# Optimization experiments

Measured on AMD Instinct MI355X. Metric: run time of the kernel, lower is better.

Reference implementation:

```python
import jax, jax.numpy as jnp
import numpy as np

B, N, INTER, RNN, W = 256, 128, 128, 128, 8


def _rms(x):
    # x / sqrt(mean(x^2, dim=2))
    return x / jnp.sqrt(jnp.mean(x * x, axis=2, keepdims=True))


def _sage(x, src, dst, deg, wl, bl, wr):
    # PyG SAGEConv(mean aggr, normalize=True): lin_l(mean_j x_j) + lin_r(x), then L2-normalize.
    # edge_index from torch.combinations(arange(k),2).t(): src=row0 (i<j), dst=row1;
    # batch repeat duplicates edges without node offsets -> mean unchanged, only nodes <N aggregate.
    agg = jax.ops.segment_sum(x[src], dst, num_segments=x.shape[0]) / deg[:, None]
    out = agg @ wl.T + bl + x @ wr.T
    nrm = jnp.maximum(jnp.linalg.norm(out, axis=-1, keepdims=True), 1e-12)
    return out / nrm


def setup_inputs() -> dict:
    key = jax.random.key(0)
    ks = jax.random.split(key, 32)
    g = lambda i, shape: jax.random.normal(ks[i], shape, dtype=jnp.float32) * 0.05
    return {
        'flows': jax.random.normal(ks[0], (B, N, N), dtype=jnp.float32),
        'coords_emb': jax.random.normal(ks[1], (B, N, 2 * N), dtype=jnp.float32),
        # Encoder_Coords: 4 pointwise Conv1d layers (kernel=1 == per-token Linear)
        'cw1': g(2, (INTER, 2 * N)), 'cb1': g(3, (INTER,)),
        'cw2': g(4, (2 * INTER, INTER)), 'cb2': g(5, (2 * INTER,)),
        'cw3': g(6, (RNN, 2 * INTER)), 'cb3': g(7, (RNN,)),
        'cw4': g(8, (RNN, RNN)), 'cb4': g(9, (RNN,)),
        # Encoder_Flows: 4 SAGEConv layers (lin_l with bias, lin_r no bias)
        'g1_wl': g(10, (INTER, N)), 'g1_bl': g(11, (INTER,)), 'g1_wr': g(12, (INTER, N)),
        'g2_wl': g(13, (2 * INTER, INTER)), 'g2_bl': g(14, (2 * INTER,)), 'g2_wr': g(15, (2 * INTER, INTER)),
        'g3_wl': g(16, (INTER, 2 * INTER)), 'g3_bl': g(17, (INTER,)), 'g3_wr': g(18, (INTER, 2 * INTER)),
        'g4_wl': g(19, (RNN, INTER)), 'g4_bl': g(20, (RNN,)), 'g4_wr': g(21, (RNN, INTER)),
        # Worker: per-worker Q/K projections (bias=False), stacked [W, out, in]
        'qca': g(22, (W, RNN, RNN)), 'kca': g(23, (W, RNN, RNN)),
        'qsa': g(24, (W, RNN, RNN)), 'ksa': g(25, (W, RNN, RNN)),
        # s_1s[0], s_2s[0]: Linear(N*W -> N, bias=False)
        's1w': g(26, (N, N * W)), 's2w': g(27, (N, N * W)),
    }


def reference(flows, coords_emb, cw1, cb1, cw2, cb2, cw3, cb3, cw4, cb4,
              g1_wl, g1_bl, g1_wr, g2_wl, g2_bl, g2_wr, g3_wl, g3_bl, g3_wr,
              g4_wl, g4_bl, g4_wr, qca, kca, qsa, ksa, s1w, s2w):
    # ---- rms_norm inputs (Model.action) ----
    f_in = _rms(flows)
    c_in = _rms(coords_emb)

    # ---- Encoder_Flows: SAGE stack over flattened [B*N, N] nodes ----
    x = f_in.reshape(-1, N)                      # [B*N, N]
    src, dst = jnp.triu_indices(N, k=1)          # combinations(arange(N), r=2)
    deg = jnp.maximum(
        jax.ops.segment_sum(jnp.ones_like(src, dtype=x.dtype), dst, num_segments=x.shape[0]), 1.0)
    x = _sage(x, src, dst, deg, g1_wl, g1_bl, g1_wr)
    x = _sage(x, src, dst, deg, g2_wl, g2_bl, g2_wr)
    x = _sage(x, src, dst, deg, g3_wl, g3_bl, g3_wr)
    x = _sage(x, src, dst, deg, g4_wl, g4_bl, g4_wr)
    f = _rms(jax.nn.relu(x).reshape(B, N, RNN))

    # ---- Encoder_Coords: 4 pointwise convs (no nonlinearity), attn=False ----
    c = c_in @ cw1.T + cb1
    c = c @ cw2.T + cb2
    c = c @ cw3.T + cb3
    c = c @ cw4.T + cb4
    c = _rms(c)

    # ---- Worker (dropout=0.0 -> identity) ----
    scale = jnp.sqrt(jnp.float32(RNN))
    # cross-attention branch (result discarded by Worker.forward, kept for fidelity)
    Qc = jnp.einsum('bnd,wod->bwno', f, qca)
    Kc = jnp.einsum('bmd,wod->bwmo', c, kca)
    ca = jnp.einsum('bwno,bwmo->bwnm', Qc, Kc) / scale
    ca = ca.transpose(0, 2, 3, 1).reshape(B, N, N * W) @ s1w.T  # [B,N,N], unused
    # self-attention branch (returned)
    Qs = jnp.einsum('bnd,wod->bwno', f, qsa)
    Ks = jnp.einsum('bmd,wod->bwmo', f, ksa)
    sa = jnp.einsum('bwno,bwmo->bwnm', Qs, Ks) / scale          # [B,W,N,N]
    sa = sa.transpose(0, 2, 3, 1).reshape(B, N, N * W) @ s2w.T  # [B,N,N]
    return sa
```

## Files before the change

kernel.cpp:

```cpp
#include <hip/hip_runtime.h>
#include <math.h>


typedef __attribute__((ext_vector_type(8))) short bf16x8;
typedef __attribute__((ext_vector_type(4))) float f32x4;

__device__ inline ushort f2b(float x) {
  unsigned u = __builtin_bit_cast(unsigned, x);
  unsigned r = (u + 0x7fffu + ((u >> 16) & 1u)) >> 16;
  return (ushort)r;
}
__device__ inline int ftswz(int e) { return ((e & 7) ^ ((e >> 3) & 15)) << 4; }

__device__ inline void ctr_signal(unsigned* c) {
  __threadfence();
  __syncthreads();
  if (threadIdx.x == 0)
    __hip_atomic_fetch_add(c, 1u, __ATOMIC_RELEASE, __HIP_MEMORY_SCOPE_AGENT);
}
__device__ inline void ctr_wait(unsigned* c, unsigned tgt) {
  if (threadIdx.x == 0) {
    while (__hip_atomic_load(c, __ATOMIC_ACQUIRE, __HIP_MEMORY_SCOPE_AGENT) < tgt)
      __builtin_amdgcn_s_sleep(8);
  }
  __syncthreads();
}

__global__ __launch_bounds__(256) void prep_all_k(
    const float* __restrict__ s2w,
    const float* __restrict__ wl1, const float* __restrict__ wl2,
    const float* __restrict__ wl3, const float* __restrict__ wl4,
    const float* __restrict__ wr1, const float* __restrict__ wr2,
    const float* __restrict__ wr3, const float* __restrict__ wr4,
    ushort* __restrict__ SBp, ushort* __restrict__ WL, ushort* __restrict__ WR,
    ushort* __restrict__ WRp, float* __restrict__ SS, unsigned* __restrict__ CTR) {
  if (blockIdx.x == 0) {
    SS[threadIdx.x] = 0.f;
    SS[threadIdx.x + 256] = 0.f;
    if (threadIdx.x < 8) CTR[threadIdx.x] = 0u;
  }
  int i = blockIdx.x * 256 + threadIdx.x;
  if (i < 131072) {
    int w = i >> 14, p = (i >> 7) & 127, m = i & 127;
    int sidx = ((((w * 2 + (p >> 6)) * 4 + ((p >> 4) & 3)) * 4 + (m >> 5)) * 64 +
                ((m >> 3) & 3) * 16 + (p & 15)) * 8 + (m & 7);
    SBp[sidx] = f2b(s2w[p * 1024 + m * 8 + w]);
    return;
  }
  i -= 131072;
  if (i < 98304) {
    float v, u;
    int base, K, col, k;
    if (i < 16384)      { v = wl1[i];         u = wr1[i];         base = 0;     K = 128; col = i >> 7;            k = i & 127; }
    else if (i < 49152) { int j = i - 16384;  v = wl2[j]; u = wr2[j]; base = 16384; K = 128; col = j >> 7;       k = j & 127; }
    else if (i < 81920) { int j = i - 49152;  v = wl3[j]; u = wr3[j]; base = 49152; K = 256; col = j >> 8;       k = j & 255; }
    else                { int j = i - 81920;  v = wl4[j]; u = wr4[j]; base = 81920; K = 128; col = j >> 7;       k = j & 127; }
    WL[i] = f2b(v);
    ushort ub = f2b(u);
    WR[i] = ub;
    int pidx = base + (((col >> 4) * (K / 32) + (k >> 5)) * 64 +
                       ((k >> 3) & 3) * 16 + (col & 15)) * 8 + (k & 7);
    WRp[pidx] = ub;
  }
}

template <int K, int N, int MODE>
__device__ void chain_dev(char* XS, char* C0T, float* sArr,
                          const float* __restrict__ flows, const ushort* __restrict__ XTsrc,
                          const float* __restrict__ SSprev,
                          const ushort* __restrict__ Wl, const ushort* __restrict__ Wr,
                          const float* __restrict__ bias,
                          ushort* __restrict__ XTdst, float* __restrict__ YTdst,
                          float* __restrict__ SScur, int cbid) {
  const int tid = threadIdx.x;
  const int lane = tid & 63, wv = tid >> 6, lr = lane & 15, lg = lane >> 4;
  const int cG0 = cbid * 16;

  if (MODE == 0) {
    #pragma unroll
    for (int it = 0; it < 16; ++it) {
      int idx = tid + it * 256;
      int row = idx >> 5, c4 = idx & 31;
      const float4 v = *reinterpret_cast<const float4*>(flows + (size_t)row * 128 + c4 * 4);
      float ss = v.x * v.x + v.y * v.y + v.z * v.z + v.w * v.w;
      ss += __shfl_xor(ss, 16); ss += __shfl_xor(ss, 8);
      ss += __shfl_xor(ss, 4);  ss += __shfl_xor(ss, 2); ss += __shfl_xor(ss, 1);
      *reinterpret_cast<ushort*>(XS + (c4 * 4 + 0) * 272 + row * 2) = f2b(v.x);
      *reinterpret_cast<ushort*>(XS + (c4 * 4 + 1) * 272 + row * 2) = f2b(v.y);
      *reinterpret_cast<ushort*>(XS + (c4 * 4 + 2) * 272 + row * 2) = f2b(v.z);
      *reinterpret_cast<ushort*>(XS + (c4 * 4 + 3) * 272 + row * 2) = f2b(v.w);
      if ((tid & 31) == 0) sArr[row] = rsqrtf(ss * (1.0f / 128.0f));
    }
  } else {
    for (int e = tid * 8; e < K * 128; e += 2048) {
      uint4 v = *reinterpret_cast<const uint4*>(XTsrc + e);
      *reinterpret_cast<uint4*>(XS + (e >> 7) * 272 + (e & 127) * 2) = v;
    }
    if (tid < 128) sArr[tid] = 1.0f / fmaxf(sqrtf(SSprev[tid]), 1e-12f);
  }
  __syncthreads();

  bf16x8 a[2][K / 32];
  float sr[2][4];
  #pragma unroll
  for (int mt = 0; mt < 2; ++mt) {
    int R = wv * 32 + mt * 16 + lr;
    #pragma unroll
    for (int ks = 0; ks < K / 32; ++ks) {
      union { ushort us[8]; bf16x8 v; } u;
      #pragma unroll
      for (int j = 0; j < 8; ++j)
        u.us[j] = *reinterpret_cast<const ushort*>(XS + (ks * 32 + lg * 8 + j) * 272 + R * 2);
      a[mt][ks] = u.v;
    }
    #pragma unroll
    for (int rr = 0; rr < 4; ++rr) sr[mt][rr] = sArr[wv * 32 + mt * 16 + 4 * lg + rr];
  }

  bf16x8 aL[2][4];
  #pragma unroll
  for (int mt = 0; mt < 2; ++mt) {
    int rowL = wv * 32 + mt * 16 + lr;
    ushort iv = f2b(1.0f / (float)(rowL > 1 ? rowL : 1));
    #pragma unroll
    for (int ks = 0; ks < 4; ++ks)
      #pragma unroll
      for (int j = 0; j < 8; ++j) {
        int k = ks * 32 + lg * 8 + j;
        aL[mt][ks][j] = (short)((k < rowL) ? iv : 0);
      }
  }

  const int cG = cG0 + lr;
  {
    bf16x8 bw[K / 32];
    #pragma unroll
    for (int ks = 0; ks < K / 32; ++ks)
      bw[ks] = *reinterpret_cast<const bf16x8*>(Wl + (size_t)cG * K + ks * 32 + lg * 8);
    #pragma unroll
    for (int mt = 0; mt < 2; ++mt) {
      f32x4 acc = {0.f, 0.f, 0.f, 0.f};
      #pragma unroll
      for (int ks = 0; ks < K / 32; ++ks)
        acc = __builtin_amdgcn_mfma_f32_16x16x32_bf16(a[mt][ks], bw[ks], acc, 0, 0, 0);
      int m0 = wv * 32 + mt * 16 + lg * 4;
      uint2 pk;
      pk.x = (unsigned)f2b(acc[0] * sr[mt][0]) | ((unsigned)f2b(acc[1] * sr[mt][1]) << 16);
      pk.y = (unsigned)f2b(acc[2] * sr[mt][2]) | ((unsigned)f2b(acc[3] * sr[mt][3]) << 16);
      *reinterpret_cast<uint2*>(C0T + lr * 256 + ((2 * m0) ^ ((lr & 7) << 4))) = pk;
    }
  }
  __syncthreads();

  {
    bf16x8 bc[4], bw[K / 32];
    #pragma unroll
    for (int ks = 0; ks < 4; ++ks)
      bc[ks] = *reinterpret_cast<const bf16x8*>(C0T + lr * 256 + ((ks * 64 + lg * 16) ^ ((lr & 7) << 4)));
    #pragma unroll
    for (int ks = 0; ks < K / 32; ++ks)
      bw[ks] = *reinterpret_cast<const bf16x8*>(Wr + (size_t)cG * K + ks * 32 + lg * 8);
    float bb = bias[cG];
    #pragma unroll
    for (int mt = 0; mt < 2; ++mt) {
      f32x4 cacc = {0.f, 0.f, 0.f, 0.f}, acc = {0.f, 0.f, 0.f, 0.f};
      #pragma unroll
      for (int ks = 0; ks < 4; ++ks)
        cacc = __builtin_amdgcn_mfma_f32_16x16x32_bf16(aL[mt][ks], bc[ks], cacc, 0, 0, 0);
      #pragma unroll
      for (int ks = 0; ks < K / 32; ++ks)
        acc = __builtin_amdgcn_mfma_f32_16x16x32_bf16(a[mt][ks], bw[ks], acc, 0, 0, 0);
      int m0 = wv * 32 + mt * 16 + lg * 4;
      float ssq[4];
      if (MODE < 2) {
        float y0 = acc[0] * sr[mt][0] + bb + cacc[0];
        float y1 = acc[1] * sr[mt][1] + bb + cacc[1];
        float y2 = acc[2] * sr[mt][2] + bb + cacc[2];
        float y3 = acc[3] * sr[mt][3] + bb + cacc[3];
        uint2 pk;
        pk.x = (unsigned)f2b(y0) | ((unsigned)f2b(y1) << 16);
        pk.y = (unsigned)f2b(y2) | ((unsigned)f2b(y3) << 16);
        *reinterpret_cast<uint2*>(&XTdst[(size_t)cG * 128 + m0]) = pk;
        ssq[0] = y0 * y0; ssq[1] = y1 * y1; ssq[2] = y2 * y2; ssq[3] = y3 * y3;
      } else {
        float4 vv;
        vv.x = fmaxf(acc[0] * sr[mt][0] + bb + cacc[0], 0.f);
        vv.y = fmaxf(acc[1] * sr[mt][1] + bb + cacc[1], 0.f);
        vv.z = fmaxf(acc[2] * sr[mt][2] + bb + cacc[2], 0.f);
        vv.w = fmaxf(acc[3] * sr[mt][3] + bb + cacc[3], 0.f);
        *reinterpret_cast<float4*>(&YTdst[(size_t)cG * 128 + m0]) = vv;
        ssq[0] = vv.x * vv.x; ssq[1] = vv.y * vv.y; ssq[2] = vv.z * vv.z; ssq[3] = vv.w * vv.w;
      }
      #pragma unroll
      for (int rr = 0; rr < 4; ++rr) {
        float ss = ssq[rr];
        ss += __shfl_xor(ss, 1); ss += __shfl_xor(ss, 2);
        ss += __shfl_xor(ss, 4); ss += __shfl_xor(ss, 8);
        if (lr == 0) atomicAdd(&SScur[m0 + rr], ss);
      }
    }
  }
}

__device__ inline void stage_flows_nb(const float* __restrict__ flows, int blk,
                                      char* A_, float* sArr, int wv, int lane) {
  int r2 = lane >> 5;
  int c4 = lane & 31;
  #pragma unroll
  for (int it = 0; it < 8; ++it) {
    int rowbase = wv * 16 + it * 2;
    const float4 v = *reinterpret_cast<const float4*>(
        flows + ((size_t)blk * 64 + rowbase) * 128 + lane * 4);
    int row = rowbase + r2;
    float ss = v.x * v.x + v.y * v.y + v.z * v.z + v.w * v.w;
    ss += __shfl_xor(ss, 16); ss += __shfl_xor(ss, 8);
    ss += __shfl_xor(ss, 4);  ss += __shfl_xor(ss, 2); ss += __shfl_xor(ss, 1);
    uint2 pk;
    pk.x = (unsigned)f2b(v.x) | ((unsigned)f2b(v.y) << 16);
    pk.y = (unsigned)f2b(v.z) | ((unsigned)f2b(v.w) << 16);
    *reinterpret_cast<uint2*>(A_ + row * 256 + ((c4 * 8) ^ ((row & 7) << 4))) = pk;
    if (c4 == 0) sArr[row] = rsqrtf(ss * (1.0f / 128.0f));
  }
}

template <int K, int N>
__device__ inline void sage_layer_nb(const char* Xsrc, char* Xdst,
                                     const float* sP, float* sN,
                                     const ushort* __restrict__ Wrp,
                                     const float* __restrict__ bias,
                                     int wv, int lr, int lg, int l64) {
  bf16x8 a[K / 32];
  float sr[4];
  int rowA = wv * 16 + lr;
  #pragma unroll
  for (int ks = 0; ks < K / 32; ++ks)
    a[ks] = *reinterpret_cast<const bf16x8*>(
        Xsrc + rowA * (K * 2) + ((ks * 64 + lg * 16) ^ ((rowA & 7) << 4)));
  #pragma unroll
  for (int rr = 0; rr < 4; ++rr) sr[rr] = sP[wv * 16 + 4 * lg + rr];
  float ssq[4] = {0.f, 0.f, 0.f, 0.f};
  #pragma unroll
  for (int nt = 0; nt < N / 16; ++nt) {
    int col = nt * 16 + lr;
    bf16x8 b[K / 32];
    #pragma unroll
    for (int ks = 0; ks < K / 32; ++ks)
      b[ks] = *reinterpret_cast<const bf16x8*>(Wrp + (((size_t)nt * (K / 32) + ks) * 64 + l64) * 8);
    f32x4 acc = {0.f, 0.f, 0.f, 0.f};
    #pragma unroll
    for (int ks = 0; ks < K / 32; ++ks)
      acc = __builtin_amdgcn_mfma_f32_16x16x32_bf16(a[ks], b[ks], acc, 0, 0, 0);
    float bb = bias[col];
    #pragma unroll
    for (int rr = 0; rr < 4; ++rr) {
      int row = wv * 16 + 4 * lg + rr;
      float y = acc[rr] * sr[rr] + bb;
      *reinterpret_cast<ushort*>(Xdst + row * (N * 2) + ((col * 2) ^ ((row & 7) << 4))) = f2b(y);
      ssq[rr] += y * y;
    }
  }
  #pragma unroll
  for (int rr = 0; rr < 4; ++rr) {
    float ss = ssq[rr];
    ss += __shfl_xor(ss, 1); ss += __shfl_xor(ss, 2);
    ss += __shfl_xor(ss, 4); ss += __shfl_xor(ss, 8);
    if (lr == 0) sN[wv * 16 + 4 * lg + rr] = 1.0f / fmaxf(sqrtf(ss), 1e-12f);
  }
}

__device__ inline void sage_layer_last_nb(const char* Xsrc, const float* sP,
                                          const ushort* __restrict__ Wrp,
                                          const float* __restrict__ bias,
                                          int wv, int lr, int lg, int l64,
                                          ushort* __restrict__ Fg, int blk) {
  bf16x8 a[4];
  float sr[4];
  int rowA = wv * 16 + lr;
  #pragma unroll
  for (int ks = 0; ks < 4; ++ks)
    a[ks] = *reinterpret_cast<const bf16x8*>(
        Xsrc + rowA * 256 + ((ks * 64 + lg * 16) ^ ((rowA & 7) << 4)));
  #pragma unroll
  for (int rr = 0; rr < 4; ++rr) sr[rr] = sP[wv * 16 + 4 * lg + rr];
  float yreg[8][4];
  float ssq[4] = {0.f, 0.f, 0.f, 0.f};
  #pragma unroll
  for (int nt = 0; nt < 8; ++nt) {
    int col = nt * 16 + lr;
    bf16x8 b[4];
    #pragma unroll
    for (int ks = 0; ks < 4; ++ks)
      b[ks] = *reinterpret_cast<const bf16x8*>(Wrp + (((size_t)nt * 4 + ks) * 64 + l64) * 8);
    f32x4 acc = {0.f, 0.f, 0.f, 0.f};
    #pragma unroll
    for (int ks = 0; ks < 4; ++ks)
      acc = __builtin_amdgcn_mfma_f32_16x16x32_bf16(a[ks], b[ks], acc, 0, 0, 0);
    float bb = bias[col];
    #pragma unroll
    for (int rr = 0; rr < 4; ++rr) {
      float y = acc[rr] * sr[rr] + bb;
      yreg[nt][rr] = y;
      float v = fmaxf(y, 0.f);
      ssq[rr] += v * v;
    }
  }
  float sc[4];
  #pragma unroll
  for (int rr = 0; rr < 4; ++rr) {
    float ss = ssq[rr];
    ss += __shfl_xor(ss, 1); ss += __shfl_xor(ss, 2);
    ss += __shfl_xor(ss, 4); ss += __shfl_xor(ss, 8);
    sc[rr] = sqrtf(128.0f / fmaxf(ss, 1e-20f));
  }
  #pragma unroll
  for (int nt = 0; nt < 8; ++nt)
    #pragma unroll
    for (int rr = 0; rr < 4; ++rr) {
      int row = wv * 16 + 4 * lg + rr;
      Fg[((size_t)blk * 64 + row) * 128 + nt * 16 + lr] = f2b(fmaxf(yreg[nt][rr], 0.f) * sc[rr]);
    }
}

__global__ __launch_bounds__(256, 2) void mega2_k(
    const float* __restrict__ flows,
    const float* __restrict__ qsa, const float* __restrict__ ksa,
    const ushort* __restrict__ WL, const ushort* __restrict__ WR,
    const ushort* __restrict__ WRp,
    const float* __restrict__ bl1, const float* __restrict__ bl2,
    const float* __restrict__ bl3, const float* __restrict__ bl4,
    ushort* __restrict__ Fg, ushort* __restrict__ MBT,
    ushort* __restrict__ XT1, ushort* __restrict__ XT2, ushort* __restrict__ XT3,
    float* __restrict__ YT4, float* __restrict__ SS, unsigned* __restrict__ CTR) {
  __shared__ char L[74240];
  const int bid = blockIdx.x;
  const int tid = threadIdx.x;
  const int lane = tid & 63, wv = tid >> 6, lr = lane & 15, lg = lane >> 4;

  if (bid < 16) {
    char* XS = L;
    char* C0T = L + 69632;
    float* sArr = (float*)(L + 73728);
    int cbid = bid;
    if (cbid < 8) {
      chain_dev<128, 128, 0>(XS, C0T, sArr, flows, nullptr, nullptr,
                             WL + 0, WR + 0, bl1, XT1, nullptr, SS + 0, cbid);
      ctr_signal(&CTR[0]);
    }
    ctr_wait(&CTR[0], 8);
    chain_dev<128, 256, 1>(XS, C0T, sArr, nullptr, XT1, SS + 0,
                           WL + 16384, WR + 16384, bl2, XT2, nullptr, SS + 128, cbid);
    ctr_signal(&CTR[1]);
    ctr_wait(&CTR[1], 16);
    if (cbid < 8) {
      chain_dev<256, 128, 1>(XS, C0T, sArr, nullptr, XT2, SS + 128,
                             WL + 49152, WR + 49152, bl3, XT3, nullptr, SS + 256, cbid);
      ctr_signal(&CTR[2]);
    }
    ctr_wait(&CTR[2], 8);
    if (cbid < 8) {
      chain_dev<128, 128, 2>(XS, C0T, sArr, nullptr, XT3, SS + 256,
                             WL + 81920, WR + 81920, bl4, nullptr, YT4, SS + 384, cbid);
      ctr_signal(&CTR[3]);
    }
    ctr_wait(&CTR[3], 8);
    if (cbid < 8) {
      int t = cbid * 256 + tid;
      int r = t >> 4, cs = t & 15;
      float sc = sqrtf(128.0f / fmaxf(SS[384 + r], 1e-20f));
      ushort tmp[8];
      #pragma unroll
      for (int j = 0; j < 8; ++j) {
        int c = cs * 8 + j;
        tmp[j] = f2b(YT4[(size_t)c * 128 + r] * sc);
      }
      *reinterpret_cast<uint4*>(&Fg[(size_t)r * 128 + cs * 8]) = *reinterpret_cast<uint4*>(tmp);
    }
    return;
  }

  if (bid < 24) {
    char* QT  = L;
    char* KTm = L + 32768;
    int w = bid - 16;
    const float* qw = qsa + (size_t)w * 16384;
    const float* kw = ksa + (size_t)w * 16384;
    for (int e = tid; e < 16384; e += 256) {
      int op = e >> 7, c = e & 127;
      int off = c * 256 + ((op * 2) ^ ((c & 7) << 4));
      *reinterpret_cast<ushort*>(QT + off)  = f2b(qw[e]);
      *reinterpret_cast<ushort*>(KTm + off) = f2b(kw[e]);
    }
    __syncthreads();
    #pragma unroll
    for (int rt = 0; rt < 2; ++rt) {
      int e = wv * 32 + rt * 16 + lr;
      bf16x8 a[4];
      #pragma unroll
      for (int ks = 0; ks < 4; ++ks)
        a[ks] = *reinterpret_cast<const bf16x8*>(KTm + e * 256 + ((ks * 64 + lg * 16) ^ ((e & 7) << 4)));
      #pragma unroll
      for (int ct = 0; ct < 8; ++ct) {
        int d = ct * 16 + lr;
        bf16x8 bq[4];
        #pragma unroll
        for (int ks = 0; ks < 4; ++ks)
          bq[ks] = *reinterpret_cast<const bf16x8*>(QT + d * 256 + ((ks * 64 + lg * 16) ^ ((d & 7) << 4)));
        f32x4 acc = {0.f, 0.f, 0.f, 0.f};
        #pragma unroll
        for (int ks = 0; ks < 4; ++ks)
          acc = __builtin_amdgcn_mfma_f32_16x16x32_bf16(a[ks], bq[ks], acc, 0, 0, 0);
        uint2 pk;
        pk.x = (unsigned)f2b(acc[0]) | ((unsigned)f2b(acc[1]) << 16);
        pk.y = (unsigned)f2b(acc[2]) | ((unsigned)f2b(acc[3]) << 16);
        size_t base = ((((size_t)ct * 8 + w) * 4 + wv) * 64 +
                       (size_t)(((rt * 2 + (lg >> 1)) & 3) * 16 + lr)) * 8 + (lg & 1) * 4;
        *reinterpret_cast<uint2*>(&MBT[base]) = pk;
      }
    }
    return;
  }

  char* A_ = L;
  char* B_ = L + 16384;
  char* C_ = L + 32768;
  float* sA = (float*)(L + 65536);
  float* sB = (float*)(L + 65792);
  const int l64 = lane;
  int blk = bid - 24 + 2;
  stage_flows_nb(flows, blk, A_, sA, wv, lane);
  asm volatile("" ::: "memory");
  sage_layer_nb<128, 128>(A_, B_, sA, sB, WRp + 0,     bl1, wv, lr, lg, l64);
  asm volatile("" ::: "memory");
  sage_layer_nb<128, 256>(B_, C_, sB, sA, WRp + 16384, bl2, wv, lr, lg, l64);
  asm volatile("" ::: "memory");
  sage_layer_nb<256, 128>(C_, A_, sA, sB, WRp + 49152, bl3, wv, lr, lg, l64);
  asm volatile("" ::: "memory");
  sage_layer_last_nb(A_, sB, WRp + 81920, bl4, wv, lr, lg, l64, Fg, blk);
}

__global__ __launch_bounds__(512, 4) void attn_fused(
    const ushort* __restrict__ F, const ushort* __restrict__ MBT,
    const ushort* __restrict__ SBp, float* __restrict__ Out) {
  __shared__ char FT[32768];
  __shared__ char RTb[32768];

  const int bq = blockIdx.x;
  const int b = bq >> 1, ph = bq & 1;
  const int tid = threadIdx.x;
  const int l = tid & 63, wv = tid >> 6;
  const int lr = l & 15, lg = l >> 4;

  const ushort* Fb = F + (size_t)b * 16384;

  #pragma unroll
  for (int it = 0; it < 4; ++it) {
    int idx = tid + it * 512;
    int m = idx >> 4, eg = idx & 15;
    uint4 v = *reinterpret_cast<const uint4*>(Fb + m * 128 + eg * 8);
    const ushort* pv = reinterpret_cast<const ushort*>(&v);
    #pragma unroll
    for (int j = 0; j < 8; ++j) {
      int e = eg * 8 + j;
      *reinterpret_cast<ushort*>(FT + e * 256 + ((m * 2) ^ ftswz(e))) = pv[j];
    }
  }

  bf16x8 fa[4];
  {
    int n = wv * 16 + lr;
    #pragma unroll
    for (int ks = 0; ks < 4; ++ks)
      fa[ks] = *reinterpret_cast<const bf16x8*>(Fb + n * 128 + ks * 32 + lg * 8);
  }
  __syncthreads();

  bf16x8 af[4];
  {
    int e = wv * 16 + lr;
    #pragma unroll
    for (int ks = 0; ks < 4; ++ks)
      af[ks] = *reinterpret_cast<const bf16x8*>(
          FT + e * 256 + ((ks * 64 + lg * 16) ^ ftswz(e)));
  }

  f32x4 zacc[4];
  #pragma unroll
  for (int pt = 0; pt < 4; ++pt) zacc[pt] = f32x4{0.f, 0.f, 0.f, 0.f};

  const int eb0 = 2 * (wv * 16 + lg * 4);

  auto Rphase = [&](int w, char* RT) {
    #pragma unroll
    for (int pt = 0; pt < 4; ++pt) {
      int p = pt * 16 + lr;
      bf16x8 bs[4];
      #pragma unroll
      for (int ks = 0; ks < 4; ++ks)
        bs[ks] = *reinterpret_cast<const bf16x8*>(
            SBp + ((((size_t)(w * 2 + ph) * 4 + pt) * 4 + ks) * 64 + l) * 8);
      f32x4 rr = {0.f, 0.f, 0.f, 0.f};
      #pragma unroll
      for (int ks = 0; ks < 4; ++ks)
        rr = __builtin_amdgcn_mfma_f32_16x16x32_bf16(af[ks], bs[ks], rr, 0, 0, 0);
      uint2 pk;
      pk.x = (unsigned)f2b(rr[0]) | ((unsigned)f2b(rr[1]) << 16);
      pk.y = (unsigned)f2b(rr[2]) | ((unsigned)f2b(rr[3]) << 16);
      *reinterpret_cast<uint2*>(RT + p * 256 + (eb0 ^ ((p & 7) << 4))) = pk;
    }
  };
  auto Zphase = [&](int w, const char* RT) {
    bf16x8 mf[4];
    #pragma unroll
    for (int ks = 0; ks < 4; ++ks)
      mf[ks] = *reinterpret_cast<const bf16x8*>(
          MBT + ((((size_t)wv * 8 + w) * 4 + ks) * 64 + l) * 8);
    #pragma unroll
    for (int pt = 0; pt < 4; ++pt) {
      int p = pt * 16 + lr;
      bf16x8 bg[4];
      #pragma unroll
      for (int ks = 0; ks < 4; ++ks)
        bg[ks] = *reinterpret_cast<const bf16x8*>(
            RT + p * 256 + ((ks * 64 + lg * 16) ^ ((p & 7) << 4)));
      #pragma unroll
      for (int ks = 0; ks < 4; ++ks)
        zacc[pt] = __builtin_amdgcn_mfma_f32_16x16x32_bf16(mf[ks], bg[ks], zacc[pt], 0, 0, 0);
    }
  };

  Rphase(0, RTb);
  __syncthreads();
  #pragma unroll
  for (int w = 0; w < 7; ++w) {
    Zphase(w, RTb + (w & 1) * 16384);
    Rphase(w + 1, RTb + ((w + 1) & 1) * 16384);
    __syncthreads();
  }
  Zphase(7, RTb + 16384);
  #pragma unroll
  for (int pt = 0; pt < 4; ++pt) {
    int p = pt * 16 + lr;
    uint2 pk;
    pk.x = (unsigned)f2b(zacc[pt][0]) | ((unsigned)f2b(zacc[pt][1]) << 16);
    pk.y = (unsigned)f2b(zacc[pt][2]) | ((unsigned)f2b(zacc[pt][3]) << 16);
    *reinterpret_cast<uint2*>(RTb + p * 256 + (eb0 ^ ((p & 7) << 4))) = pk;
  }
  __syncthreads();

  const float inv_scale = 0.08838834764831845f;
  float* ob = Out + (size_t)b * 16384 + ph * 64;
  #pragma unroll
  for (int pt = 0; pt < 4; ++pt) {
    int p = pt * 16 + lr;
    bf16x8 bz[4];
    #pragma unroll
    for (int ks = 0; ks < 4; ++ks)
      bz[ks] = *reinterpret_cast<const bf16x8*>(
          RTb + p * 256 + ((ks * 64 + lg * 16) ^ ((p & 7) << 4)));
    f32x4 oa = {0.f, 0.f, 0.f, 0.f};
    #pragma unroll
    for (int ks = 0; ks < 4; ++ks)
      oa = __builtin_amdgcn_mfma_f32_16x16x32_bf16(fa[ks], bz[ks], oa, 0, 0, 0);
    int n0 = wv * 16 + lg * 4;
    #pragma unroll
    for (int r = 0; r < 4; ++r)
      ob[(size_t)(n0 + r) * 128 + p] = oa[r] * inv_scale;
  }
}

extern "C" void kernel_launch(void* const* d_in, const int* in_sizes, int n_in,
                              void* d_out, int out_size, void* d_ws, size_t ws_size,
                              hipStream_t stream) {
  const float* flows = (const float*)d_in[0];
  const float* g1_wl = (const float*)d_in[10];
  const float* g1_bl = (const float*)d_in[11];
  const float* g1_wr = (const float*)d_in[12];
  const float* g2_wl = (const float*)d_in[13];
  const float* g2_bl = (const float*)d_in[14];
  const float* g2_wr = (const float*)d_in[15];
  const float* g3_wl = (const float*)d_in[16];
  const float* g3_bl = (const float*)d_in[17];
  const float* g3_wr = (const float*)d_in[18];
  const float* g4_wl = (const float*)d_in[19];
  const float* g4_bl = (const float*)d_in[20];
  const float* g4_wr = (const float*)d_in[21];
  const float* qsa   = (const float*)d_in[24];
  const float* ksa   = (const float*)d_in[25];
  const float* s2w   = (const float*)d_in[27];
  float* out = (float*)d_out;
  char* wsb  = (char*)d_ws;

  ushort* FB16 = (ushort*)(wsb);
  ushort* SBp  = (ushort*)(wsb + 8388608);
  ushort* WL   = (ushort*)(wsb + 8650752);
  ushort* WR   = (ushort*)(wsb + 8847360);
  ushort* MBT  = (ushort*)(wsb + 9043968);
  ushort* XT1  = (ushort*)(wsb + 9306112);
  ushort* XT2  = (ushort*)(wsb + 9338880);
  ushort* XT3  = (ushort*)(wsb + 9404416);
  float*  YT4  = (float*)(wsb + 9437184);
  float*  SS   = (float*)(wsb + 9502720);
  ushort* WRp  = (ushort*)(wsb + 9504768);
  unsigned* CTR = (unsigned*)(wsb + 9701376);

  prep_all_k<<<896, 256, 0, stream>>>(s2w,
                                      g1_wl, g2_wl, g3_wl, g4_wl,
                                      g1_wr, g2_wr, g3_wr, g4_wr,
                                      SBp, WL, WR, WRp, SS, CTR);
  mega2_k<<<534, 256, 0, stream>>>(flows, qsa, ksa, WL, WR, WRp,
                                   g1_bl, g2_bl, g3_bl, g4_bl,
                                   FB16, MBT, XT1, XT2, XT3, YT4, SS, CTR);
  attn_fused<<<512, 512, 0, stream>>>(FB16, MBT, SBp, out);
}
```

Before: 86.75 us.

## Cut mega kernel shared memory to fit three blocks per CU

```diff
diff --git a/kernel.cpp b/kernel.cpp
--- a/kernel.cpp
+++ b/kernel.cpp
@@ -11,6 +11,7 @@
   return (ushort)r;
 }
 __device__ inline int ftswz(int e) { return ((e & 7) ^ ((e >> 3) & 15)) << 4; }
+__device__ inline int cAddrRow(int rl) { return (rl < 8) ? rl * 512 : 8192 + (rl - 8) * 512; }
 
 __device__ inline void ctr_signal(unsigned* c) {
   __threadfence();
@@ -74,47 +75,67 @@
                           float* __restrict__ SScur, int cbid) {
   const int tid = threadIdx.x;
   const int lane = tid & 63, wv = tid >> 6, lr = lane & 15, lg = lane >> 4;
-  const int cG0 = cbid * 16;
-
-  if (MODE == 0) {
-    #pragma unroll
-    for (int it = 0; it < 16; ++it) {
-      int idx = tid + it * 256;
-      int row = idx >> 5, c4 = idx & 31;
-      const float4 v = *reinterpret_cast<const float4*>(flows + (size_t)row * 128 + c4 * 4);
-      float ss = v.x * v.x + v.y * v.y + v.z * v.z + v.w * v.w;
-      ss += __shfl_xor(ss, 16); ss += __shfl_xor(ss, 8);
-      ss += __shfl_xor(ss, 4);  ss += __shfl_xor(ss, 2); ss += __shfl_xor(ss, 1);
-      *reinterpret_cast<ushort*>(XS + (c4 * 4 + 0) * 272 + row * 2) = f2b(v.x);
-      *reinterpret_cast<ushort*>(XS + (c4 * 4 + 1) * 272 + row * 2) = f2b(v.y);
-      *reinterpret_cast<ushort*>(XS + (c4 * 4 + 2) * 272 + row * 2) = f2b(v.z);
-      *reinterpret_cast<ushort*>(XS + (c4 * 4 + 3) * 272 + row * 2) = f2b(v.w);
-      if ((tid & 31) == 0) sArr[row] = rsqrtf(ss * (1.0f / 128.0f));
-    }
-  } else {
-    for (int e = tid * 8; e < K * 128; e += 2048) {
-      uint4 v = *reinterpret_cast<const uint4*>(XTsrc + e);
-      *reinterpret_cast<uint4*>(XS + (e >> 7) * 272 + (e & 127) * 2) = v;
-    }
-    if (tid < 128) sArr[tid] = 1.0f / fmaxf(sqrtf(SSprev[tid]), 1e-12f);
-  }
-  __syncthreads();
-
-  bf16x8 a[2][K / 32];
+  const int cG = cbid * 16 + lr;
+  constexpr int NH = K / 128;
+
   float sr[2][4];
-  #pragma unroll
-  for (int mt = 0; mt < 2; ++mt) {
-    int R = wv * 32 + mt * 16 + lr;
-    #pragma unroll
-    for (int ks = 0; ks < K / 32; ++ks) {
-      union { ushort us[8]; bf16x8 v; } u;
-      #pragma unroll
-      for (int j = 0; j < 8; ++j)
-        u.us[j] = *reinterpret_cast<const ushort*>(XS + (ks * 32 + lg * 8 + j) * 272 + R * 2);
-      a[mt][ks] = u.v;
-    }
-    #pragma unroll
-    for (int rr = 0; rr < 4; ++rr) sr[mt][rr] = sArr[wv * 32 + mt * 16 + 4 * lg + rr];
+  f32x4 acc1[2] = {{0.f,0.f,0.f,0.f},{0.f,0.f,0.f,0.f}};
+  f32x4 acc2[2] = {{0.f,0.f,0.f,0.f},{0.f,0.f,0.f,0.f}};
+
+  #pragma unroll
+  for (int h = 0; h < NH; ++h) {
+    __syncthreads();
+    if (MODE == 0) {
+      #pragma unroll
+      for (int it = 0; it < 16; ++it) {
+        int idx = tid + it * 256;
+        int row = idx >> 5, c4 = idx & 31;
+        const float4 v = *reinterpret_cast<const float4*>(flows + (size_t)row * 128 + c4 * 4);
+        float ss = v.x * v.x + v.y * v.y + v.z * v.z + v.w * v.w;
+        ss += __shfl_xor(ss, 16); ss += __shfl_xor(ss, 8);
+        ss += __shfl_xor(ss, 4);  ss += __shfl_xor(ss, 2); ss += __shfl_xor(ss, 1);
+        *reinterpret_cast<ushort*>(XS + (c4 * 4 + 0) * 272 + row * 2) = f2b(v.x);
+        *reinterpret_cast<ushort*>(XS + (c4 * 4 + 1) * 272 + row * 2) = f2b(v.y);
+        *reinterpret_cast<ushort*>(XS + (c4 * 4 + 2) * 272 + row * 2) = f2b(v.z);
+        *reinterpret_cast<ushort*>(XS + (c4 * 4 + 3) * 272 + row * 2) = f2b(v.w);
+        if ((tid & 31) == 0) sArr[row] = rsqrtf(ss * (1.0f / 128.0f));
+      }
+    } else {
+      for (int e = tid * 8; e < 16384; e += 2048) {
+        uint4 v = *reinterpret_cast<const uint4*>(XTsrc + h * 16384 + e);
+        *reinterpret_cast<uint4*>(XS + (e >> 7) * 272 + (e & 127) * 2) = v;
+      }
+      if (h == 0 && tid < 128) sArr[tid] = 1.0f / fmaxf(sqrtf(SSprev[tid]), 1e-12f);
+    }
+    __syncthreads();
+
+    #pragma unroll
+    for (int mt = 0; mt < 2; ++mt) {
+      int R = wv * 32 + mt * 16 + lr;
+      bf16x8 a[4];
+      #pragma unroll
+      for (int ks = 0; ks < 4; ++ks) {
+        union { ushort us[8]; bf16x8 v; } u;
+        #pragma unroll
+        for (int j = 0; j < 8; ++j)
+          u.us[j] = *reinterpret_cast<const ushort*>(XS + (ks * 32 + lg * 8 + j) * 272 + R * 2);
+        a[ks] = u.v;
+      }
+      if (h == 0) {
+        #pragma unroll
+        for (int rr = 0; rr < 4; ++rr) sr[mt][rr] = sArr[wv * 32 + mt * 16 + 4 * lg + rr];
+      }
+      #pragma unroll
+      for (int ks = 0; ks < 4; ++ks) {
+        bf16x8 bw = *reinterpret_cast<const bf16x8*>(Wl + (size_t)cG * K + h * 128 + ks * 32 + lg * 8);
+        acc1[mt] = __builtin_amdgcn_mfma_f32_16x16x32_bf16(a[ks], bw, acc1[mt], 0, 0, 0);
+      }
+      #pragma unroll
+      for (int ks = 0; ks < 4; ++ks) {
+        bf16x8 bw = *reinterpret_cast<const bf16x8*>(Wr + (size_t)cG * K + h * 128 + ks * 32 + lg * 8);
+        acc2[mt] = __builtin_amdgcn_mfma_f32_16x16x32_bf16(a[ks], bw, acc2[mt], 0, 0, 0);
+      }
+    }
   }
 
   bf16x8 aL[2][4];
@@ -131,52 +152,35 @@
       }
   }
 
-  const int cG = cG0 + lr;
+  #pragma unroll
+  for (int mt = 0; mt < 2; ++mt) {
+    int m0 = wv * 32 + mt * 16 + lg * 4;
+    uint2 pk;
+    pk.x = (unsigned)f2b(acc1[mt][0] * sr[mt][0]) | ((unsigned)f2b(acc1[mt][1] * sr[mt][1]) << 16);
+    pk.y = (unsigned)f2b(acc1[mt][2] * sr[mt][2]) | ((unsigned)f2b(acc1[mt][3] * sr[mt][3]) << 16);
+    *reinterpret_cast<uint2*>(C0T + lr * 256 + ((2 * m0) ^ ((lr & 7) << 4))) = pk;
+  }
+  __syncthreads();
+
   {
-    bf16x8 bw[K / 32];
-    #pragma unroll
-    for (int ks = 0; ks < K / 32; ++ks)
-      bw[ks] = *reinterpret_cast<const bf16x8*>(Wl + (size_t)cG * K + ks * 32 + lg * 8);
+    bf16x8 bc[4];
+    #pragma unroll
+    for (int ks = 0; ks < 4; ++ks)
+      bc[ks] = *reinterpret_cast<const bf16x8*>(C0T + lr * 256 + ((ks * 64 + lg * 16) ^ ((lr & 7) << 4)));
+    float bb = (MODE < 2) ? bias[cG] : bias[cG];
     #pragma unroll
     for (int mt = 0; mt < 2; ++mt) {
-      f32x4 acc = {0.f, 0.f, 0.f, 0.f};
-      #pragma unroll
-      for (int ks = 0; ks < K / 32; ++ks)
-        acc = __builtin_amdgcn_mfma_f32_16x16x32_bf16(a[mt][ks], bw[ks], acc, 0, 0, 0);
-      int m0 = wv * 32 + mt * 16 + lg * 4;
-      uint2 pk;
-      pk.x = (unsigned)f2b(acc[0] * sr[mt][0]) | ((unsigned)f2b(acc[1] * sr[mt][1]) << 16);
-      pk.y = (unsigned)f2b(acc[2] * sr[mt][2]) | ((unsigned)f2b(acc[3] * sr[mt][3]) << 16);
-      *reinterpret_cast<uint2*>(C0T + lr * 256 + ((2 * m0) ^ ((lr & 7) << 4))) = pk;
-    }
-  }
-  __syncthreads();
-
-  {
-    bf16x8 bc[4], bw[K / 32];
-    #pragma unroll
-    for (int ks = 0; ks < 4; ++ks)
-      bc[ks] = *reinterpret_cast<const bf16x8*>(C0T + lr * 256 + ((ks * 64 + lg * 16) ^ ((lr & 7) << 4)));
-    #pragma unroll
-    for (int ks = 0; ks < K / 32; ++ks)
-      bw[ks] = *reinterpret_cast<const bf16x8*>(Wr + (size_t)cG * K + ks * 32 + lg * 8);
-    float bb = bias[cG];
-    #pragma unroll
-    for (int mt = 0; mt < 2; ++mt) {
-      f32x4 cacc = {0.f, 0.f, 0.f, 0.f}, acc = {0.f, 0.f, 0.f, 0.f};
+      f32x4 cacc = {0.f, 0.f, 0.f, 0.f};
       #pragma unroll
       for (int ks = 0; ks < 4; ++ks)
         cacc = __builtin_amdgcn_mfma_f32_16x16x32_bf16(aL[mt][ks], bc[ks], cacc, 0, 0, 0);
-      #pragma unroll
-      for (int ks = 0; ks < K / 32; ++ks)
-        acc = __builtin_amdgcn_mfma_f32_16x16x32_bf16(a[mt][ks], bw[ks], acc, 0, 0, 0);
       int m0 = wv * 32 + mt * 16 + lg * 4;
       float ssq[4];
       if (MODE < 2) {
-        float y0 = acc[0] * sr[mt][0] + bb + cacc[0];
-        float y1 = acc[1] * sr[mt][1] + bb + cacc[1];
-        float y2 = acc[2] * sr[mt][2] + bb + cacc[2];
-        float y3 = acc[3] * sr[mt][3] + bb + cacc[3];
+        float y0 = acc2[mt][0] * sr[mt][0] + bb + cacc[0];
+        float y1 = acc2[mt][1] * sr[mt][1] + bb + cacc[1];
+        float y2 = acc2[mt][2] * sr[mt][2] + bb + cacc[2];
+        float y3 = acc2[mt][3] * sr[mt][3] + bb + cacc[3];
         uint2 pk;
         pk.x = (unsigned)f2b(y0) | ((unsigned)f2b(y1) << 16);
         pk.y = (unsigned)f2b(y2) | ((unsigned)f2b(y3) << 16);
@@ -184,10 +188,10 @@
         ssq[0] = y0 * y0; ssq[1] = y1 * y1; ssq[2] = y2 * y2; ssq[3] = y3 * y3;
       } else {
         float4 vv;
-        vv.x = fmaxf(acc[0] * sr[mt][0] + bb + cacc[0], 0.f);
-        vv.y = fmaxf(acc[1] * sr[mt][1] + bb + cacc[1], 0.f);
-        vv.z = fmaxf(acc[2] * sr[mt][2] + bb + cacc[2], 0.f);
-        vv.w = fmaxf(acc[3] * sr[mt][3] + bb + cacc[3], 0.f);
+        vv.x = fmaxf(acc2[mt][0] * sr[mt][0] + bb + cacc[0], 0.f);
+        vv.y = fmaxf(acc2[mt][1] * sr[mt][1] + bb + cacc[1], 0.f);
+        vv.z = fmaxf(acc2[mt][2] * sr[mt][2] + bb + cacc[2], 0.f);
+        vv.w = fmaxf(acc2[mt][3] * sr[mt][3] + bb + cacc[3], 0.f);
         *reinterpret_cast<float4*>(&YTdst[(size_t)cG * 128 + m0]) = vv;
         ssq[0] = vv.x * vv.x; ssq[1] = vv.y * vv.y; ssq[2] = vv.z * vv.z; ssq[3] = vv.w * vv.w;
       }
@@ -202,60 +206,59 @@
   }
 }
 
-__device__ inline void stage_flows_nb(const float* __restrict__ flows, int blk,
-                                      char* A_, float* sArr, int wv, int lane) {
+__device__ inline void sage_stage(const float* __restrict__ flows, int blk,
+                                  char* W, float* sArr, int wv, int lane) {
   int r2 = lane >> 5;
   int c4 = lane & 31;
   #pragma unroll
   for (int it = 0; it < 8; ++it) {
-    int rowbase = wv * 16 + it * 2;
+    int rl0 = it * 2;
     const float4 v = *reinterpret_cast<const float4*>(
-        flows + ((size_t)blk * 64 + rowbase) * 128 + lane * 4);
-    int row = rowbase + r2;
+        flows + ((size_t)blk * 64 + wv * 16 + rl0) * 128 + lane * 4);
+    int rl = rl0 + r2;
     float ss = v.x * v.x + v.y * v.y + v.z * v.z + v.w * v.w;
     ss += __shfl_xor(ss, 16); ss += __shfl_xor(ss, 8);
     ss += __shfl_xor(ss, 4);  ss += __shfl_xor(ss, 2); ss += __shfl_xor(ss, 1);
     uint2 pk;
     pk.x = (unsigned)f2b(v.x) | ((unsigned)f2b(v.y) << 16);
     pk.y = (unsigned)f2b(v.z) | ((unsigned)f2b(v.w) << 16);
-    *reinterpret_cast<uint2*>(A_ + row * 256 + ((c4 * 8) ^ ((row & 7) << 4))) = pk;
-    if (c4 == 0) sArr[row] = rsqrtf(ss * (1.0f / 128.0f));
-  }
-}
-
-template <int K, int N>
-__device__ inline void sage_layer_nb(const char* Xsrc, char* Xdst,
-                                     const float* sP, float* sN,
-                                     const ushort* __restrict__ Wrp,
-                                     const float* __restrict__ bias,
-                                     int wv, int lr, int lg, int l64) {
-  bf16x8 a[K / 32];
+    *reinterpret_cast<uint2*>(W + rl * 256 + ((c4 * 8) ^ ((rl & 7) << 4))) = pk;
+    if (c4 == 0) sArr[wv * 16 + rl] = rsqrtf(ss * (1.0f / 128.0f));
+  }
+}
+
+template <int N, int DSTC>
+__device__ inline void sage_l128(const char* src, char* dstW,
+                                 const float* sP, float* sN,
+                                 const ushort* __restrict__ Wrp,
+                                 const float* __restrict__ bias,
+                                 int wv, int lr, int lg, int l64) {
+  bf16x8 a[4];
   float sr[4];
-  int rowA = wv * 16 + lr;
-  #pragma unroll
-  for (int ks = 0; ks < K / 32; ++ks)
-    a[ks] = *reinterpret_cast<const bf16x8*>(
-        Xsrc + rowA * (K * 2) + ((ks * 64 + lg * 16) ^ ((rowA & 7) << 4)));
+  #pragma unroll
+  for (int ks = 0; ks < 4; ++ks)
+    a[ks] = *reinterpret_cast<const bf16x8*>(src + lr * 256 + ((ks * 64 + lg * 16) ^ ((lr & 7) << 4)));
   #pragma unroll
   for (int rr = 0; rr < 4; ++rr) sr[rr] = sP[wv * 16 + 4 * lg + rr];
   float ssq[4] = {0.f, 0.f, 0.f, 0.f};
   #pragma unroll
   for (int nt = 0; nt < N / 16; ++nt) {
     int col = nt * 16 + lr;
-    bf16x8 b[K / 32];
-    #pragma unroll
-    for (int ks = 0; ks < K / 32; ++ks)
-      b[ks] = *reinterpret_cast<const bf16x8*>(Wrp + (((size_t)nt * (K / 32) + ks) * 64 + l64) * 8);
+    bf16x8 b[4];
+    #pragma unroll
+    for (int ks = 0; ks < 4; ++ks)
+      b[ks] = *reinterpret_cast<const bf16x8*>(Wrp + (((size_t)nt * 4 + ks) * 64 + l64) * 8);
     f32x4 acc = {0.f, 0.f, 0.f, 0.f};
     #pragma unroll
-    for (int ks = 0; ks < K / 32; ++ks)
+    for (int ks = 0; ks < 4; ++ks)
       acc = __builtin_amdgcn_mfma_f32_16x16x32_bf16(a[ks], b[ks], acc, 0, 0, 0);
     float bb = bias[col];
     #pragma unroll
     for (int rr = 0; rr < 4; ++rr) {
-      int row = wv * 16 + 4 * lg + rr;
+      int rl = 4 * lg + rr;
       float y = acc[rr] * sr[rr] + bb;
-      *reinterpret_cast<ushort*>(Xdst + row * (N * 2) + ((col * 2) ^ ((row & 7) << 4))) = f2b(y);
+      int rowbase = DSTC ? cAddrRow(rl) : rl * 256;
+      *reinterpret_cast<ushort*>(dstW + rowbase + ((col * 2) ^ ((rl & 7) << 4))) = f2b(y);
       ssq[rr] += y * y;
     }
   }
@@ -268,18 +271,56 @@
   }
 }
 
-__device__ inline void sage_layer_last_nb(const char* Xsrc, const float* sP,
-                                          const ushort* __restrict__ Wrp,
-                                          const float* __restrict__ bias,
-                                          int wv, int lr, int lg, int l64,
-                                          ushort* __restrict__ Fg, int blk) {
+__device__ inline void sage_l3(const char* W, char* dstD,
+                               const float* sP, float* sN,
+                               const ushort* __restrict__ Wrp,
+                               const float* __restrict__ bias,
+                               int wv, int lr, int lg, int l64) {
+  bf16x8 a[8];
+  float sr[4];
+  #pragma unroll
+  for (int ks = 0; ks < 8; ++ks)
+    a[ks] = *reinterpret_cast<const bf16x8*>(W + cAddrRow(lr) + ((ks * 64 + lg * 16) ^ ((lr & 7) << 4)));
+  #pragma unroll
+  for (int rr = 0; rr < 4; ++rr) sr[rr] = sP[wv * 16 + 4 * lg + rr];
+  float ssq[4] = {0.f, 0.f, 0.f, 0.f};
+  #pragma unroll
+  for (int nt = 0; nt < 8; ++nt) {
+    int col = nt * 16 + lr;
+    f32x4 acc = {0.f, 0.f, 0.f, 0.f};
+    #pragma unroll
+    for (int ks = 0; ks < 8; ++ks) {
+      bf16x8 b = *reinterpret_cast<const bf16x8*>(Wrp + (((size_t)nt * 8 + ks) * 64 + l64) * 8);
+      acc = __builtin_amdgcn_mfma_f32_16x16x32_bf16(a[ks], b, acc, 0, 0, 0);
+    }
+    float bb = bias[col];
+    #pragma unroll
+    for (int rr = 0; rr < 4; ++rr) {
+      int rl = 4 * lg + rr;
+      float y = acc[rr] * sr[rr] + bb;
+      *reinterpret_cast<ushort*>(dstD + rl * 256 + ((col * 2) ^ ((rl & 7) << 4))) = f2b(y);
+      ssq[rr] += y * y;
+    }
+  }
+  #pragma unroll
+  for (int rr = 0; rr < 4; ++rr) {
+    float ss = ssq[rr];
+    ss += __shfl_xor(ss, 1); ss += __shfl_xor(ss, 2);
+    ss += __shfl_xor(ss, 4); ss += __shfl_xor(ss, 8);
+    if (lr == 0) sN[wv * 16 + 4 * lg + rr] = 1.0f / fmaxf(sqrtf(ss), 1e-12f);
+  }
+}
+
+__device__ inline void sage_l4(const char* src, const float* sP,
+                               const ushort* __restrict__ Wrp,
+                               const float* __restrict__ bias,
+                               int wv, int lr, int lg, int l64,
+                               ushort* __restrict__ Fg, int blk) {
   bf16x8 a[4];
   float sr[4];
-  int rowA = wv * 16 + lr;
   #pragma unroll
   for (int ks = 0; ks < 4; ++ks)
-    a[ks] = *reinterpret_cast<const bf16x8*>(
-        Xsrc + rowA * 256 + ((ks * 64 + lg * 16) ^ ((rowA & 7) << 4)));
+    a[ks] = *reinterpret_cast<const bf16x8*>(src + lr * 256 + ((ks * 64 + lg * 16) ^ ((lr & 7) << 4)));
   #pragma unroll
   for (int rr = 0; rr < 4; ++rr) sr[rr] = sP[wv * 16 + 4 * lg + rr];
   float yreg[8][4];
@@ -321,7 +362,7 @@
     }
 }
 
-__global__ __launch_bounds__(256, 2) void mega2_k(
+__global__ __launch_bounds__(256, 3) void mega3_k(
     const float* __restrict__ flows,
     const float* __restrict__ qsa, const float* __restrict__ ksa,
     const ushort* __restrict__ WL, const ushort* __restrict__ WR,
@@ -331,15 +372,15 @@
     ushort* __restrict__ Fg, ushort* __restrict__ MBT,
     ushort* __restrict__ XT1, ushort* __restrict__ XT2, ushort* __restrict__ XT3,
     float* __restrict__ YT4, float* __restrict__ SS, unsigned* __restrict__ CTR) {
-  __shared__ char L[74240];
+  __shared__ char L[49664];
   const int bid = blockIdx.x;
   const int tid = threadIdx.x;
   const int lane = tid & 63, wv = tid >> 6, lr = lane & 15, lg = lane >> 4;
 
   if (bid < 16) {
     char* XS = L;
-    char* C0T = L + 69632;
-    float* sArr = (float*)(L + 73728);
+    char* C0T = L + 34816;
+    float* sArr = (float*)(L + 38912);
     int cbid = bid;
     if (cbid < 8) {
       chain_dev<128, 128, 0>(XS, C0T, sArr, flows, nullptr, nullptr,
@@ -379,16 +420,14 @@
   }
 
   if (bid < 24) {
-    char* QT  = L;
-    char* KTm = L + 32768;
+    char* QT = L;
     int w = bid - 16;
     const float* qw = qsa + (size_t)w * 16384;
     const float* kw = ksa + (size_t)w * 16384;
     for (int e = tid; e < 16384; e += 256) {
       int op = e >> 7, c = e & 127;
       int off = c * 256 + ((op * 2) ^ ((c & 7) << 4));
-      *reinterpret_cast<ushort*>(QT + off)  = f2b(qw[e]);
-      *reinterpret_cast<ushort*>(KTm + off) = f2b(kw[e]);
+      *reinterpret_cast<ushort*>(QT + off) = f2b(qw[e]);
     }
     __syncthreads();
     #pragma unroll
@@ -396,8 +435,13 @@
       int e = wv * 32 + rt * 16 + lr;
       bf16x8 a[4];
       #pragma unroll
-      for (int ks = 0; ks < 4; ++ks)
-        a[ks] = *reinterpret_cast<const bf16x8*>(KTm + e * 256 + ((ks * 64 + lg * 16) ^ ((e & 7) << 4)));
+      for (int ks = 0; ks < 4; ++ks) {
+        union { ushort us[8]; bf16x8 v; } u;
+        #pragma unroll
+        for (int j = 0; j < 8; ++j)
+          u.us[j] = f2b(kw[(size_t)(ks * 32 + lg * 8 + j) * 128 + e]);
+        a[ks] = u.v;
+      }
       #pragma unroll
       for (int ct = 0; ct < 8; ++ct) {
         int d = ct * 16 + lr;
@@ -420,22 +464,20 @@
     return;
   }
 
-  char* A_ = L;
-  char* B_ = L + 16384;
-  char* C_ = L + 32768;
-  float* sA = (float*)(L + 65536);
-  float* sB = (float*)(L + 65792);
+  char* W = L + wv * 12288;
+  float* sA = (float*)(L + 49152);
+  float* sB = (float*)(L + 49408);
   const int l64 = lane;
   int blk = bid - 24 + 2;
-  stage_flows_nb(flows, blk, A_, sA, wv, lane);
+  sage_stage(flows, blk, W, sA, wv, lane);
   asm volatile("" ::: "memory");
-  sage_layer_nb<128, 128>(A_, B_, sA, sB, WRp + 0,     bl1, wv, lr, lg, l64);
+  sage_l128<128, 0>(W, W + 4096, sA, sB, WRp + 0,     bl1, wv, lr, lg, l64);
   asm volatile("" ::: "memory");
-  sage_layer_nb<128, 256>(B_, C_, sB, sA, WRp + 16384, bl2, wv, lr, lg, l64);
+  sage_l128<256, 1>(W + 4096, W, sB, sA, WRp + 16384, bl2, wv, lr, lg, l64);
   asm volatile("" ::: "memory");
-  sage_layer_nb<256, 128>(C_, A_, sA, sB, WRp + 49152, bl3, wv, lr, lg, l64);
+  sage_l3(W, W + 4096, sA, sB, WRp + 49152, bl3, wv, lr, lg, l64);
   asm volatile("" ::: "memory");
-  sage_layer_last_nb(A_, sB, WRp + 81920, bl4, wv, lr, lg, l64, Fg, blk);
+  sage_l4(W + 4096, sB, WRp + 81920, bl4, wv, lr, lg, l64, Fg, blk);
 }
 
 __global__ __launch_bounds__(512, 4) void attn_fused(
@@ -607,7 +649,7 @@
                                       g1_wl, g2_wl, g3_wl, g4_wl,
                                       g1_wr, g2_wr, g3_wr, g4_wr,
                                       SBp, WL, WR, WRp, SS, CTR);
-  mega2_k<<<534, 256, 0, stream>>>(flows, qsa, ksa, WL, WR, WRp,
+  mega3_k<<<534, 256, 0, stream>>>(flows, qsa, ksa, WL, WR, WRp,
                                    g1_bl, g2_bl, g3_bl, g4_bl,
                                    FB16, MBT, XT1, XT2, XT3, YT4, SS, CTR);
   attn_fused<<<512, 512, 0, stream>>>(FB16, MBT, SBp, out);
```

After: 96.67 us. +11.4%, slower.
